# Performance work log

Measured on AMD Instinct MI355X. Metric: run time of the kernel, lower is better.

## Reference

```python
import jax, jax.numpy as jnp
import numpy as np

EMBED = 384
HEADS = 7
HEAD_SIZE = EMBED // HEADS  # 54; concat dim = 378 != 384 (faithful to source)
SEQ = 512
BATCH = 64
FFN = 6 * EMBED
EPS = 1e-5


def _layernorm(x, g, b):
    mu = jnp.mean(x, axis=-1, keepdims=True)
    var = jnp.mean((x - mu) ** 2, axis=-1, keepdims=True)
    return (x - mu) * jax.lax.rsqrt(var + EPS) * g + b


def setup_inputs() -> dict:
    key = jax.random.key(0)
    ks = jax.random.split(key, 14)
    s = 0.02
    return {
        "x": jax.random.normal(ks[0], (BATCH, SEQ, EMBED), jnp.float32),
        # per-head q/k/v projections stacked over heads: [H, EMBED, HEAD_SIZE]
        "wq": jax.random.normal(ks[1], (HEADS, EMBED, HEAD_SIZE), jnp.float32) * s,
        "bq": jnp.zeros((HEADS, HEAD_SIZE), jnp.float32),
        "wk": jax.random.normal(ks[2], (HEADS, EMBED, HEAD_SIZE), jnp.float32) * s,
        "bk": jnp.zeros((HEADS, HEAD_SIZE), jnp.float32),
        "wv": jax.random.normal(ks[3], (HEADS, EMBED, HEAD_SIZE), jnp.float32) * s,
        "bv": jnp.zeros((HEADS, HEAD_SIZE), jnp.float32),
        "wo": jax.random.normal(ks[4], (HEADS * HEAD_SIZE, EMBED), jnp.float32) * s,
        "bo": jnp.zeros((EMBED,), jnp.float32),
        "w1": jax.random.normal(ks[5], (EMBED, FFN), jnp.float32) * s,
        "b1": jnp.zeros((FFN,), jnp.float32),
        "w2": jax.random.normal(ks[6], (FFN, EMBED), jnp.float32) * s,
        "b2": jnp.zeros((EMBED,), jnp.float32),
        "ln1_g": jnp.ones((EMBED,), jnp.float32),
        "ln1_b": jnp.zeros((EMBED,), jnp.float32),
        "ln2_g": jnp.ones((EMBED,), jnp.float32),
        "ln2_b": jnp.zeros((EMBED,), jnp.float32),
    }


def reference(x, wq, bq, wk, bk, wv, bv, wo, bo, w1, b1, w2, b2, ln1_g, ln1_b, ln2_g, ln2_b):
    B, S, D = x.shape
    # --- multi-head causal self-attention (pre-LN) ---
    h = _layernorm(x, ln1_g, ln1_b)
    q = jnp.einsum("bsd,hdk->bhsk", h, wq) + bq[None, :, None, :]
    k = jnp.einsum("bsd,hdk->bhsk", h, wk) + bk[None, :, None, :]
    v = jnp.einsum("bsd,hdk->bhsk", h, wv) + bv[None, :, None, :]
    scale = HEAD_SIZE ** -0.5
    scores = jnp.einsum("bhsk,bhtk->bhst", q, k) * scale  # [B,H,S,S]
    causal = jnp.tril(jnp.ones((S, S), dtype=bool))
    scores = jnp.where(causal, scores, jnp.float32(-jnp.inf))
    attn = jax.nn.softmax(scores, axis=-1)
    o = jnp.einsum("bhst,bhtk->bhsk", attn, v)  # [B,H,S,hs]
    o = jnp.transpose(o, (0, 2, 1, 3)).reshape(B, S, HEADS * HEAD_SIZE)
    x = x + o @ wo + bo  # dropout = identity (eval)
    # --- feed-forward (pre-LN), exact GELU ---
    h2 = _layernorm(x, ln2_g, ln2_b)
    ff = jax.nn.gelu(h2 @ w1 + b1, approximate=False) @ w2 + b2
    return x + ff
```

## Files before the change

### kernel.cpp

```cpp
#include <hip/hip_runtime.h>
#include <hip/hip_bf16.h>
#include <cmath>

#define BATCH 64
#define SEQ   512
#define EMBED 384
#define HEADS 7
#define HSZ   54
#define FFND  2304
#define NTOK  (BATCH*SEQ)
#define QKVN  1152
#define EPS   1e-5f
#define SCALE 0.13608276348795434f

typedef __attribute__((ext_vector_type(8))) short s16x8;
typedef __attribute__((ext_vector_type(4))) float f32x4;

__device__ __forceinline__ ushort f2bf(float f) {
  __hip_bfloat16 h = __float2bfloat16(f);
  return *reinterpret_cast<ushort*>(&h);
}

__device__ __forceinline__ void gload16(const void* g, void* l) {
  __builtin_amdgcn_global_load_lds((const __attribute__((address_space(1))) void*)g,
                                   (__attribute__((address_space(3))) void*)l, 16, 0, 0);
}

__global__ __launch_bounds__(256) void ln_bf16_kernel(const float* __restrict__ x,
    const float* __restrict__ g, const float* __restrict__ b, ushort* __restrict__ out) {
  int wave = threadIdx.x >> 6, lane = threadIdx.x & 63;
  int row = (blockIdx.x << 2) + wave;
  const float* xr = x + (size_t)row * EMBED;
  float v[6]; float s = 0.f;
#pragma unroll
  for (int i = 0; i < 6; ++i) { v[i] = xr[lane + (i << 6)]; s += v[i]; }
#pragma unroll
  for (int off = 32; off; off >>= 1) s += __shfl_xor(s, off);
  float mu = s * (1.f / EMBED);
  float var = 0.f;
#pragma unroll
  for (int i = 0; i < 6; ++i) { float d = v[i] - mu; var += d * d; }
#pragma unroll
  for (int off = 32; off; off >>= 1) var += __shfl_xor(var, off);
  float rstd = rsqrtf(var * (1.f / EMBED) + EPS);
  ushort* orow = out + (size_t)row * EMBED;
#pragma unroll
  for (int i = 0; i < 6; ++i) {
    int c = lane + (i << 6);
    orow[c] = f2bf((v[i] - mu) * rstd * g[c] + b[c]);
  }
}

__global__ __launch_bounds__(256) void convT_tiled(const float* __restrict__ in,
    ushort* __restrict__ out, int K, int N, int srcK, int srcN) {
  __shared__ float t[32][33];
  int k0 = blockIdx.x << 5, n0 = blockIdx.y << 5;
  int tx = threadIdx.x & 31, ty = threadIdx.x >> 5;
#pragma unroll
  for (int i = 0; i < 4; ++i) {
    int r = ty + i * 8;
    int k = k0 + r, n = n0 + tx;
    t[r][tx] = (k < srcK && n < srcN) ? in[(size_t)k * srcN + n] : 0.f;
  }
  __syncthreads();
#pragma unroll
  for (int i = 0; i < 4; ++i) {
    int r = ty + i * 8;
    int n = n0 + r, k = k0 + tx;
    if (n < N && k < K) out[(size_t)n * K + k] = f2bf(t[tx][r]);
  }
}

__global__ __launch_bounds__(256) void conv_qkvw_tiled(const float* __restrict__ wq,
    const float* __restrict__ wk, const float* __restrict__ wv, ushort* __restrict__ wt) {
  __shared__ float t[32][33];
  int k0 = blockIdx.x << 5, hs0 = blockIdx.y << 5;
  int z = blockIdx.z, type = z / 7, h = z - type * 7;
  const float* W = (type == 0) ? wq : (type == 1) ? wk : wv;
  int tx = threadIdx.x & 31, ty = threadIdx.x >> 5;
#pragma unroll
  for (int i = 0; i < 4; ++i) {
    int r = ty + i * 8;
    int k = k0 + r, hs = hs0 + tx;
    t[r][tx] = (hs < HSZ) ? W[((size_t)h * EMBED + k) * HSZ + hs] : 0.f;
  }
  __syncthreads();
#pragma unroll
  for (int i = 0; i < 4; ++i) {
    int r = ty + i * 8;
    int hs = hs0 + r, k = k0 + tx;
    if (hs < HSZ) wt[(size_t)(type * 378 + h * HSZ + hs) * EMBED + k0 + tx] = f2bf(t[tx][r]);
  }
}

__global__ __launch_bounds__(256) void fill_misc(const float* __restrict__ bq,
    const float* __restrict__ bk, const float* __restrict__ bv,
    ushort* __restrict__ wt, float* __restrict__ bqkv) {
  int idx = blockIdx.x * 256 + threadIdx.x;
  if (idx < 18 * EMBED) wt[1134 * EMBED + idx] = 0;
  if (idx < QKVN) {
    float bval = 0.f;
    if (idx < 1134) {
      int type = idx / 378, rem = idx - type * 378;
      int h = rem / HSZ, hs = rem - h * HSZ;
      const float* B = (type == 0) ? bq : (type == 1) ? bk : bv;
      bval = B[h * HSZ + hs];
    }
    bqkv[idx] = bval;
  }
}

__global__ __launch_bounds__(256) void pad_aout_kernel(ushort* __restrict__ aout) {
  int idx = blockIdx.x * 256 + threadIdx.x;
  if (idx >= NTOK * 6) return;
  int row = idx / 6, c = idx - row * 6;
  aout[(size_t)row * EMBED + 378 + c] = 0;
}

__global__ __launch_bounds__(256) void attn_mfma_kernel(const ushort* __restrict__ qkv,
    ushort* __restrict__ o) {
  __shared__ ushort Ks[2][4096];
  __shared__ ushort Vt[2][4096];
  int tid = threadIdx.x;
  int id = blockIdx.x;
  int xcd = id & 7;
  int sseq = id >> 3;
  int bh = xcd + 8 * (sseq >> 3);
  int qt = (SEQ / 64 - 1) - (sseq & 7);
  int b = bh / HEADS, h = bh - b * HEADS;
  int qr0 = qt << 6;
  int w = tid >> 6, l = tid & 63;
  int lr = l & 15, lg = l >> 4;
  const ushort* base = qkv + (size_t)b * SEQ * QKVN + h * HSZ;
  const size_t TSTR = (size_t)64 * QKVN * 2;

  int grow = w * 8 + (l >> 3);
  int gc = (l & 7) ^ (l >> 3);
  const char* kg0 = (const char*)(base + 378 + (size_t)grow * QKVN + gc * 8);
  const char* kg1 = (const char*)(base + 378 + (size_t)(grow + 32) * QKVN + gc * 8);
  const char* qg0 = (const char*)(base + (size_t)(qr0 + grow) * QKVN + gc * 8);
  const char* qg1 = (const char*)(base + (size_t)(qr0 + grow + 32) * QKVN + gc * 8);
  int vdst[7]; const char* vsrc[7]; bool vpar[7];
#pragma unroll
  for (int i = 0; i < 7; ++i) {
    int e = tid + i * 256;
    int ev = e >> 1, par = e & 1;
    int p = ev / 28, cv = ev - p * 28;
    if (cv < 27) {
      int k0 = 2 * p;
      int s0 = ((k0 >> 5) << 5) | (((k0 >> 2) & 3) << 3) | (((k0 >> 4) & 1) << 2) | (k0 & 3);
      int d = 2 * cv + par;
      vdst[i] = d * 64 + (s0 ^ ((d & 7) << 3));
      vsrc[i] = (const char*)(base + 756 + (size_t)(2 * p + par) * QKVN + 2 * cv);
      vpar[i] = (par != 0);
    } else { vdst[i] = -1; vsrc[i] = (const char*)base; vpar[i] = false; }
  }

  gload16(qg0, (char*)&Ks[1][0] + w * 1024);
  gload16(qg1, (char*)&Ks[1][0] + 4096 + w * 1024);
  gload16(kg0, (char*)&Ks[0][0] + w * 1024);
  gload16(kg1, (char*)&Ks[0][0] + 4096 + w * 1024);
  uint uv[7];
#pragma unroll
  for (int i = 0; i < 7; ++i)
    uv[i] = (vdst[i] >= 0) ? *reinterpret_cast<const uint*>(vsrc[i]) : 0u;
  __syncthreads();
  for (int e = tid; e < 320; e += 256) {
    int r = e / 5, which = e - r * 5;
    int idx = (which == 0) ? (r * 64 + ((6 ^ (r & 7)) << 3) + 6)
                           : (r * 64 + ((7 ^ (r & 7)) << 3) + 2 * (which - 1));
    *reinterpret_cast<uint*>(&Ks[1][idx]) = 0;
  }
#pragma unroll
  for (int i = 0; i < 7; ++i) {
    uint u = uv[i]; uint uo = __shfl_xor(u, 1);
    if (vdst[i] >= 0) {
      uint wv2 = vpar[i] ? ((uo >> 16) | (u & 0xffff0000u)) : ((u & 0xffffu) | (uo << 16));
      *reinterpret_cast<uint*>(&Vt[0][vdst[i]]) = wv2;
    }
  }
  __syncthreads();
  int qrow = w * 16 + lr;
  s16x8 qf[2];
  qf[0] = *reinterpret_cast<const s16x8*>(&Ks[1][qrow * 64 + ((8 * lg) ^ ((qrow & 7) << 3))]);
  qf[1] = *reinterpret_cast<const s16x8*>(&Ks[1][qrow * 64 + ((32 + 8 * lg) ^ ((qrow & 7) << 3))]);
  __syncthreads();

  int qglob = qr0 + qrow;
  float mrow = -1e30f, lrow = 0.f;
  f32x4 acc[4];
#pragma unroll
  for (int d = 0; d < 4; ++d) acc[d] = (f32x4){0.f, 0.f, 0.f, 0.f};

  for (int kt = 0; kt <= qt; ++kt) {
    int cur = kt & 1, nxt = cur ^ 1;
    if (kt < qt) {
      kg0 += TSTR; kg1 += TSTR;
      gload16(kg0, (char*)&Ks[nxt][0] + w * 1024);
      gload16(kg1, (char*)&Ks[nxt][0] + 4096 + w * 1024);
#pragma unroll
      for (int i = 0; i < 7; ++i) {
        vsrc[i] += TSTR;
        if (vdst[i] >= 0) uv[i] = *reinterpret_cast<const uint*>(vsrc[i]);
      }
    }
    f32x4 sacc[4];
    __builtin_amdgcn_s_setprio(1);
#pragma unroll
    for (int kb = 0; kb < 4; ++kb) {
      sacc[kb] = (f32x4){0.f, 0.f, 0.f, 0.f};
#pragma unroll
      for (int h2 = 0; h2 < 2; ++h2) {
        int row = kb * 16 + lr;
        s16x8 kf = *reinterpret_cast<const s16x8*>(
            &Ks[cur][row * 64 + ((32 * h2 + 8 * lg) ^ ((row & 7) << 3))]);
        sacc[kb] = __builtin_amdgcn_mfma_f32_16x16x32_bf16(kf, qf[h2], sacc[kb], 0, 0, 0);
      }
    }
    __builtin_amdgcn_s_setprio(0);
    float sv[4][4];
    float mt = -1e30f;
    bool diag = (kt == qt);
#pragma unroll
    for (int kb = 0; kb < 4; ++kb)
#pragma unroll
      for (int r = 0; r < 4; ++r) {
        float s = sacc[kb][r] * SCALE;
        if (diag && (kt * 64 + kb * 16 + 4 * lg + r) > qglob) s = -1e30f;
        sv[kb][r] = s;
        mt = fmaxf(mt, s);
      }
    mt = fmaxf(mt, __shfl_xor(mt, 16));
    mt = fmaxf(mt, __shfl_xor(mt, 32));
    if (!__all(mt - mrow <= 8.f)) {
      float mnew = fmaxf(mrow, mt);
      float al = __expf(mrow - mnew);
#pragma unroll
      for (int d = 0; d < 4; ++d)
#pragma unroll
        for (int r = 0; r < 4; ++r) acc[d][r] *= al;
      lrow *= al;
      mrow = mnew;
    }
    union { short s[16]; s16x8 v[2]; } pp;
    float lsum = 0.f;
#pragma unroll
    for (int kb = 0; kb < 4; ++kb)
#pragma unroll
      for (int r = 0; r < 4; ++r) {
        float p = __expf(sv[kb][r] - mrow);
        lsum += p;
        pp.s[kb * 4 + r] = (short)f2bf(p);
      }
    lrow += lsum;
    __builtin_amdgcn_s_setprio(1);
#pragma unroll
    for (int m = 0; m < 2; ++m)
#pragma unroll
      for (int d = 0; d < 4; ++d) {
        int row = d * 16 + lr;
        s16x8 vf = *reinterpret_cast<const s16x8*>(
            &Vt[cur][row * 64 + ((32 * m + 8 * lg) ^ ((row & 7) << 3))]);
        acc[d] = __builtin_amdgcn_mfma_f32_16x16x32_bf16(vf, pp.v[m], acc[d], 0, 0, 0);
      }
    __builtin_amdgcn_s_setprio(0);
    if (kt < qt) {
#pragma unroll
      for (int i = 0; i < 7; ++i) {
        uint u = uv[i]; uint uo = __shfl_xor(u, 1);
        if (vdst[i] >= 0) {
          uint wv2 = vpar[i] ? ((uo >> 16) | (u & 0xffff0000u)) : ((u & 0xffffu) | (uo << 16));
          *reinterpret_cast<uint*>(&Vt[nxt][vdst[i]]) = wv2;
        }
      }
      __syncthreads();
    }
  }

  lrow += __shfl_xor(lrow, 16);
  lrow += __shfl_xor(lrow, 32);
  float linv = 1.f / lrow;
  __syncthreads();
  ushort* Olds = &Ks[0][0];
#pragma unroll
  for (int d = 0; d < 4; ++d)
#pragma unroll
    for (int r = 0; r < 4; ++r)
      Olds[(d * 16 + 4 * lg + r) * 64 + w * 16 + lr] = f2bf(acc[d][r] * linv);
  __syncthreads();
  for (int e = tid; e < 64 * 27; e += 256) {
    int q = e / 27, c = e - q * 27;
    uint lo = Olds[(2 * c) * 64 + q];
    uint hi = Olds[(2 * c + 1) * 64 + q];
    *reinterpret_cast<uint*>(&o[(size_t)(b * SEQ + qr0 + q) * EMBED + h * HSZ + 2 * c]) =
        lo | (hi << 16);
  }
}

template<int KSTEPS, int LDA, int LDB, int MODE, int NY>
__global__ __launch_bounds__(256) void mfma_gemm(
    const char* __restrict__ Ab, const char* __restrict__ Btb,
    const float* __restrict__ bias, const float* __restrict__ resid,
    char* __restrict__ Cb, int ncols) {
  __shared__ ushort sh[32768];
  int tid = threadIdx.x;
  int id = blockIdx.x;
  int xcd = id & 7, t = id >> 3;
  int group = t / (4 * NY), rres = t - group * (4 * NY);
  int ytile = rres >> 2, xi = rres & 3;
  int tok0 = (xcd * 32 + group * 4 + xi) << 7;
  int col0 = ytile << 7;
  int wv = tid >> 6, l = tid & 63;
  int wr = wv >> 1, wc = wv & 1;
  int lr = l & 15, lg = l >> 4;

  const char* aptr[4]; const char* bptr[4];
#pragma unroll
  for (int is = 0; is < 4; ++is) {
    int i = is * 256 + tid;
    int row = i >> 3;
    int boff = (i & 7) << 4;
    int sw = boff ^ ((row & 7) << 4);
    aptr[is] = Ab + (size_t)(tok0 + row) * LDA + sw;
    bptr[is] = Btb + (size_t)(col0 + row) * LDB + sw;
  }

  int offA[2][4], offB[2][4];
#pragma unroll
  for (int m = 0; m < 4; ++m) {
    int rowa = wr * 64 + m * 16 + lr;
    int rowb = wc * 64 + m * 16 + lr;
    int sa = (rowa & 7) << 4, sb = (rowb & 7) << 4;
#pragma unroll
    for (int kk = 0; kk < 2; ++kk) {
      int kb = kk * 64 + lg * 16;
      offA[kk][m] = (rowa * 128 + (kb ^ sa)) >> 1;
      offB[kk][m] = (rowb * 128 + (kb ^ sb)) >> 1;
    }
  }

  f32x4 acc[4][4];
#pragma unroll
  for (int m = 0; m < 4; ++m)
#pragma unroll
    for (int n = 0; n < 4; ++n) acc[m][n] = (f32x4){0.f, 0.f, 0.f, 0.f};

#pragma unroll
  for (int is = 0; is < 4; ++is) {
    gload16(aptr[is], (char*)sh + is * 4096 + wv * 1024);
    gload16(bptr[is], (char*)sh + 32768 + is * 4096 + wv * 1024);
  }
  __syncthreads();

  for (int ks = 0; ks < KSTEPS; ++ks) {
    int buf = ks & 1;
    if (ks + 1 < KSTEPS) {
      int nb = buf ^ 1;
#pragma unroll
      for (int is = 0; is < 4; ++is) {
        gload16(aptr[is] + (size_t)(ks + 1) * 128, (char*)sh + nb * 16384 + is * 4096 + wv * 1024);
        gload16(bptr[is] + (size_t)(ks + 1) * 128, (char*)sh + 32768 + nb * 16384 + is * 4096 + wv * 1024);
      }
    }
    int ao = buf * 8192, bo = 16384 + buf * 8192;
    __builtin_amdgcn_s_setprio(1);
#pragma unroll
    for (int kk = 0; kk < 2; ++kk) {
      s16x8 af[4], bfr[4];
#pragma unroll
      for (int m = 0; m < 4; ++m) af[m] = *reinterpret_cast<const s16x8*>(&sh[ao + offA[kk][m]]);
#pragma unroll
      for (int n = 0; n < 4; ++n) bfr[n] = *reinterpret_cast<const s16x8*>(&sh[bo + offB[kk][n]]);
#pragma unroll
      for (int m = 0; m < 4; ++m)
#pragma unroll
        for (int n = 0; n < 4; ++n)
          acc[m][n] = __builtin_amdgcn_mfma_f32_16x16x32_bf16(af[m], bfr[n], acc[m][n], 0, 0, 0);
    }
    __builtin_amdgcn_s_setprio(0);
    if (ks + 1 < KSTEPS) __syncthreads();
  }

  float bn[4];
  int colr = col0 + wc * 64 + lr;
#pragma unroll
  for (int n = 0; n < 4; ++n) bn[n] = bias[colr + n * 16];

  if constexpr (MODE == 2) {
    int tokr = tok0 + wr * 64 + lg * 4;
    float* C = (float*)Cb;
#pragma unroll
    for (int m = 0; m < 4; ++m)
#pragma unroll
      for (int r = 0; r < 4; ++r) {
        size_t rowbase = (size_t)(tokr + m * 16 + r) * ncols;
#pragma unroll
        for (int n = 0; n < 4; ++n) {
          size_t idx = rowbase + colr + n * 16;
          C[idx] = acc[m][n][r] + bn[n] + resid[idx];
        }
      }
  } else {
    __syncthreads();
#pragma unroll
    for (int m = 0; m < 4; ++m)
#pragma unroll
      for (int r = 0; r < 4; ++r) {
        int row = wr * 64 + m * 16 + lg * 4 + r;
        int rmask = ((row >> 2) & 3) << 4;
#pragma unroll
        for (int n = 0; n < 4; ++n) {
          float xg = acc[m][n][r] + bn[n];
          if constexpr (MODE == 1) {
            float u2 = xg * (1.5957691216f + 0.0713548162f * xg * xg);
            xg = xg * __builtin_amdgcn_rcpf(1.f + __expf(-u2));
          }
          int col = wc * 64 + n * 16 + lr;
          sh[row * 128 + (col ^ rmask)] = f2bf(xg);
        }
      }
    __syncthreads();
    ushort* C = (ushort*)Cb;
    int blk = (l & 7) + 8 * (wv & 1);
    int rbase = (l >> 3) + 64 * (wv >> 1);
#pragma unroll
    for (int it = 0; it < 8; ++it) {
      int row = rbase + 8 * it;
      int pblk = blk ^ (((row >> 2) & 3) << 1);
      uint4 vvv = *reinterpret_cast<const uint4*>(&sh[row * 128 + pblk * 8]);
      *reinterpret_cast<uint4*>(&C[(size_t)(tok0 + row) * ncols + col0 + blk * 8]) = vvv;
    }
  }
}

extern "C" void kernel_launch(void* const* d_in, const int* in_sizes, int n_in,
                              void* d_out, int out_size, void* d_ws, size_t ws_size,
                              hipStream_t stream) {
  const float* x    = (const float*)d_in[0];
  const float* wq   = (const float*)d_in[1];
  const float* bq   = (const float*)d_in[2];
  const float* wk   = (const float*)d_in[3];
  const float* bk   = (const float*)d_in[4];
  const float* wv   = (const float*)d_in[5];
  const float* bv   = (const float*)d_in[6];
  const float* wo   = (const float*)d_in[7];
  const float* bo   = (const float*)d_in[8];
  const float* w1   = (const float*)d_in[9];
  const float* b1   = (const float*)d_in[10];
  const float* w2   = (const float*)d_in[11];
  const float* b2   = (const float*)d_in[12];
  const float* ln1g = (const float*)d_in[13];
  const float* ln1b = (const float*)d_in[14];
  const float* ln2g = (const float*)d_in[15];
  const float* ln2b = (const float*)d_in[16];
  float* out = (float*)d_out;

  char* wsb = (char*)d_ws;
  float*  x1    = (float*)wsb;
  ushort* ffnb  = (ushort*)(wsb + 50331648);
  ushort* hb    = (ushort*)(wsb + 50331648);
  ushort* qkvb  = (ushort*)(wsb + 75497472);
  ushort* aout  = (ushort*)(wsb + 150994944);
  ushort* h2b   = (ushort*)(wsb + 201326592);
  ushort* w1t   = (ushort*)(wsb + 226492416);
  ushort* w2t   = (ushort*)(wsb + 228261888);
  ushort* wqkvt = (ushort*)(wsb + 230031360);
  ushort* wot   = (ushort*)(wsb + 230916096);
  float*  bqkv  = (float*)(wsb + 231211008);

  conv_qkvw_tiled<<<dim3(12, 2, 21), 256, 0, stream>>>(wq, wk, wv, wqkvt);
  fill_misc      <<<27, 256, 0, stream>>>(bq, bk, bv, wqkvt, bqkv);
  convT_tiled    <<<dim3(12, 12), 256, 0, stream>>>(wo, wot, EMBED, EMBED, 378, EMBED);
  convT_tiled    <<<dim3(12, 72), 256, 0, stream>>>(w1, w1t, EMBED, FFND, EMBED, FFND);
  convT_tiled    <<<dim3(72, 12), 256, 0, stream>>>(w2, w2t, FFND, EMBED, FFND, EMBED);
  pad_aout_kernel<<<(NTOK * 6 + 255) / 256, 256, 0, stream>>>(aout);

  ln_bf16_kernel<<<NTOK / 4, 256, 0, stream>>>(x, ln1g, ln1b, hb);
  mfma_gemm<EMBED / 64, EMBED * 2, EMBED * 2, 0, QKVN / 128>
      <<<256 * (QKVN / 128), 256, 0, stream>>>(
      (const char*)hb, (const char*)wqkvt, bqkv, nullptr, (char*)qkvb, QKVN);
  attn_mfma_kernel<<<BATCH * HEADS * (SEQ / 64), 256, 0, stream>>>(qkvb, aout);
  mfma_gemm<EMBED / 64, EMBED * 2, EMBED * 2, 2, EMBED / 128>
      <<<256 * (EMBED / 128), 256, 0, stream>>>(
      (const char*)aout, (const char*)wot, bo, x, (char*)x1, EMBED);
  ln_bf16_kernel<<<NTOK / 4, 256, 0, stream>>>(x1, ln2g, ln2b, h2b);
  mfma_gemm<EMBED / 64, EMBED * 2, EMBED * 2, 1, FFND / 128>
      <<<256 * (FFND / 128), 256, 0, stream>>>(
      (const char*)h2b, (const char*)w1t, b1, nullptr, (char*)ffnb, FFND);
  mfma_gemm<FFND / 64, FFND * 2, FFND * 2, 2, EMBED / 128>
      <<<256 * (EMBED / 128), 256, 0, stream>>>(
      (const char*)ffnb, (const char*)w2t, b2, x1, (char*)out, EMBED);
}
```

Before: 385.8 us.

## Use 128-row query blocks with 512-thread attention blocks sharing K/V tiles

Each attention block now handles 128 query rows with 8 waves instead of 64 rows with 4 waves, so every K/V tile loaded into shared memory serves twice as many queries. Q moves to its own LDS buffer, and waves whose rows lie entirely before a key tile skip that tile's compute. This halves global K/V traffic per query and the number of blocks. In exchange it adds some causal imbalance between waves inside a block and uses more LDS and threads per block, which may lower occupancy.

New measurement: 383.0 us. No clear change (-0.7%).

```diff
diff --git a/kernel.cpp b/kernel.cpp
--- a/kernel.cpp
+++ b/kernel.cpp
@@ -117,18 +117,20 @@
   aout[(size_t)row * EMBED + 378 + c] = 0;
 }
 
-__global__ __launch_bounds__(256) void attn_mfma_kernel(const ushort* __restrict__ qkv,
+__global__ __launch_bounds__(512) void attn_mfma_kernel(const ushort* __restrict__ qkv,
     ushort* __restrict__ o) {
+  __shared__ ushort Qsh[8192];
   __shared__ ushort Ks[2][4096];
   __shared__ ushort Vt[2][4096];
   int tid = threadIdx.x;
   int id = blockIdx.x;
   int xcd = id & 7;
   int sseq = id >> 3;
-  int bh = xcd + 8 * (sseq >> 3);
-  int qt = (SEQ / 64 - 1) - (sseq & 7);
+  int bh = xcd + 8 * (sseq >> 2);
+  int qb = 3 - (sseq & 3);
   int b = bh / HEADS, h = bh - b * HEADS;
-  int qr0 = qt << 6;
+  int qr0 = qb << 7;
+  int ntile = 2 * qb + 2;
   int w = tid >> 6, l = tid & 63;
   int lr = l & 15, lg = l >> 4;
   const ushort* base = qkv + (size_t)b * SEQ * QKVN + h * HSZ;
@@ -136,17 +138,16 @@
 
   int grow = w * 8 + (l >> 3);
   int gc = (l & 7) ^ (l >> 3);
-  const char* kg0 = (const char*)(base + 378 + (size_t)grow * QKVN + gc * 8);
-  const char* kg1 = (const char*)(base + 378 + (size_t)(grow + 32) * QKVN + gc * 8);
+  const char* kg  = (const char*)(base + 378 + (size_t)grow * QKVN + gc * 8);
   const char* qg0 = (const char*)(base + (size_t)(qr0 + grow) * QKVN + gc * 8);
-  const char* qg1 = (const char*)(base + (size_t)(qr0 + grow + 32) * QKVN + gc * 8);
-  int vdst[7]; const char* vsrc[7]; bool vpar[7];
-#pragma unroll
-  for (int i = 0; i < 7; ++i) {
-    int e = tid + i * 256;
+  const char* qg1 = (const char*)(base + (size_t)(qr0 + 64 + grow) * QKVN + gc * 8);
+  int vdst[4]; const char* vsrc[4]; bool vpar[4];
+#pragma unroll
+  for (int i = 0; i < 4; ++i) {
+    int e = tid + i * 512;
     int ev = e >> 1, par = e & 1;
     int p = ev / 28, cv = ev - p * 28;
-    if (cv < 27) {
+    if (cv < 27 && p < 32) {
       int k0 = 2 * p;
       int s0 = ((k0 >> 5) << 5) | (((k0 >> 2) & 3) << 3) | (((k0 >> 4) & 1) << 2) | (k0 & 3);
       int d = 2 * cv + par;
@@ -156,23 +157,22 @@
     } else { vdst[i] = -1; vsrc[i] = (const char*)base; vpar[i] = false; }
   }
 
-  gload16(qg0, (char*)&Ks[1][0] + w * 1024);
-  gload16(qg1, (char*)&Ks[1][0] + 4096 + w * 1024);
-  gload16(kg0, (char*)&Ks[0][0] + w * 1024);
-  gload16(kg1, (char*)&Ks[0][0] + 4096 + w * 1024);
-  uint uv[7];
-#pragma unroll
-  for (int i = 0; i < 7; ++i)
+  gload16(qg0, (char*)Qsh + w * 1024);
+  gload16(qg1, (char*)Qsh + 8192 + w * 1024);
+  gload16(kg, (char*)&Ks[0][0] + w * 1024);
+  uint uv[4];
+#pragma unroll
+  for (int i = 0; i < 4; ++i)
     uv[i] = (vdst[i] >= 0) ? *reinterpret_cast<const uint*>(vsrc[i]) : 0u;
   __syncthreads();
-  for (int e = tid; e < 320; e += 256) {
+  for (int e = tid; e < 640; e += 512) {
     int r = e / 5, which = e - r * 5;
     int idx = (which == 0) ? (r * 64 + ((6 ^ (r & 7)) << 3) + 6)
                            : (r * 64 + ((7 ^ (r & 7)) << 3) + 2 * (which - 1));
-    *reinterpret_cast<uint*>(&Ks[1][idx]) = 0;
-  }
-#pragma unroll
-  for (int i = 0; i < 7; ++i) {
+    *reinterpret_cast<uint*>(&Qsh[idx]) = 0;
+  }
+#pragma unroll
+  for (int i = 0; i < 4; ++i) {
     uint u = uv[i]; uint uo = __shfl_xor(u, 1);
     if (vdst[i] >= 0) {
       uint wv2 = vpar[i] ? ((uo >> 16) | (u & 0xffff0000u)) : ((u & 0xffffu) | (uo << 16));
@@ -182,9 +182,8 @@
   __syncthreads();
   int qrow = w * 16 + lr;
   s16x8 qf[2];
-  qf[0] = *reinterpret_cast<const s16x8*>(&Ks[1][qrow * 64 + ((8 * lg) ^ ((qrow & 7) << 3))]);
-  qf[1] = *reinterpret_cast<const s16x8*>(&Ks[1][qrow * 64 + ((32 + 8 * lg) ^ ((qrow & 7) << 3))]);
-  __syncthreads();
+  qf[0] = *reinterpret_cast<const s16x8*>(&Qsh[qrow * 64 + ((8 * lg) ^ ((qrow & 7) << 3))]);
+  qf[1] = *reinterpret_cast<const s16x8*>(&Qsh[qrow * 64 + ((32 + 8 * lg) ^ ((qrow & 7) << 3))]);
 
   int qglob = qr0 + qrow;
   float mrow = -1e30f, lrow = 0.f;
@@ -192,81 +191,83 @@
 #pragma unroll
   for (int d = 0; d < 4; ++d) acc[d] = (f32x4){0.f, 0.f, 0.f, 0.f};
 
-  for (int kt = 0; kt <= qt; ++kt) {
+  for (int kt = 0; kt < ntile; ++kt) {
     int cur = kt & 1, nxt = cur ^ 1;
-    if (kt < qt) {
-      kg0 += TSTR; kg1 += TSTR;
-      gload16(kg0, (char*)&Ks[nxt][0] + w * 1024);
-      gload16(kg1, (char*)&Ks[nxt][0] + 4096 + w * 1024);
-#pragma unroll
-      for (int i = 0; i < 7; ++i) {
+    if (kt + 1 < ntile) {
+      kg += TSTR;
+      gload16(kg, (char*)&Ks[nxt][0] + w * 1024);
+#pragma unroll
+      for (int i = 0; i < 4; ++i) {
         vsrc[i] += TSTR;
         if (vdst[i] >= 0) uv[i] = *reinterpret_cast<const uint*>(vsrc[i]);
       }
     }
-    f32x4 sacc[4];
-    __builtin_amdgcn_s_setprio(1);
-#pragma unroll
-    for (int kb = 0; kb < 4; ++kb) {
-      sacc[kb] = (f32x4){0.f, 0.f, 0.f, 0.f};
-#pragma unroll
-      for (int h2 = 0; h2 < 2; ++h2) {
-        int row = kb * 16 + lr;
-        s16x8 kf = *reinterpret_cast<const s16x8*>(
-            &Ks[cur][row * 64 + ((32 * h2 + 8 * lg) ^ ((row & 7) << 3))]);
-        sacc[kb] = __builtin_amdgcn_mfma_f32_16x16x32_bf16(kf, qf[h2], sacc[kb], 0, 0, 0);
-      }
-    }
-    __builtin_amdgcn_s_setprio(0);
-    float sv[4][4];
-    float mt = -1e30f;
-    bool diag = (kt == qt);
-#pragma unroll
-    for (int kb = 0; kb < 4; ++kb)
-#pragma unroll
-      for (int r = 0; r < 4; ++r) {
-        float s = sacc[kb][r] * SCALE;
-        if (diag && (kt * 64 + kb * 16 + 4 * lg + r) > qglob) s = -1e30f;
-        sv[kb][r] = s;
-        mt = fmaxf(mt, s);
-      }
-    mt = fmaxf(mt, __shfl_xor(mt, 16));
-    mt = fmaxf(mt, __shfl_xor(mt, 32));
-    if (!__all(mt - mrow <= 8.f)) {
-      float mnew = fmaxf(mrow, mt);
-      float al = __expf(mrow - mnew);
-#pragma unroll
-      for (int d = 0; d < 4; ++d)
-#pragma unroll
-        for (int r = 0; r < 4; ++r) acc[d][r] *= al;
-      lrow *= al;
-      mrow = mnew;
-    }
-    union { short s[16]; s16x8 v[2]; } pp;
-    float lsum = 0.f;
-#pragma unroll
-    for (int kb = 0; kb < 4; ++kb)
-#pragma unroll
-      for (int r = 0; r < 4; ++r) {
-        float p = __expf(sv[kb][r] - mrow);
-        lsum += p;
-        pp.s[kb * 4 + r] = (short)f2bf(p);
-      }
-    lrow += lsum;
-    __builtin_amdgcn_s_setprio(1);
-#pragma unroll
-    for (int m = 0; m < 2; ++m)
-#pragma unroll
-      for (int d = 0; d < 4; ++d) {
-        int row = d * 16 + lr;
-        s16x8 vf = *reinterpret_cast<const s16x8*>(
-            &Vt[cur][row * 64 + ((32 * m + 8 * lg) ^ ((row & 7) << 3))]);
-        acc[d] = __builtin_amdgcn_mfma_f32_16x16x32_bf16(vf, pp.v[m], acc[d], 0, 0, 0);
-      }
-    __builtin_amdgcn_s_setprio(0);
-    if (kt < qt) {
-#pragma unroll
-      for (int i = 0; i < 7; ++i) {
+    bool active = (kt * 64) <= (qr0 + w * 16 + 15);
+    if (active) {
+      bool diag = (kt * 64 + 63) > (qr0 + w * 16);
+      f32x4 sacc[4];
+      __builtin_amdgcn_s_setprio(1);
+#pragma unroll
+      for (int kb = 0; kb < 4; ++kb) {
+        sacc[kb] = (f32x4){0.f, 0.f, 0.f, 0.f};
+#pragma unroll
+        for (int h2 = 0; h2 < 2; ++h2) {
+          int row = kb * 16 + lr;
+          s16x8 kf = *reinterpret_cast<const s16x8*>(
+              &Ks[cur][row * 64 + ((32 * h2 + 8 * lg) ^ ((row & 7) << 3))]);
+          sacc[kb] = __builtin_amdgcn_mfma_f32_16x16x32_bf16(kf, qf[h2], sacc[kb], 0, 0, 0);
+        }
+      }
+      __builtin_amdgcn_s_setprio(0);
+      float sv[4][4];
+      float mt = -1e30f;
+#pragma unroll
+      for (int kb = 0; kb < 4; ++kb)
+#pragma unroll
+        for (int r = 0; r < 4; ++r) {
+          float s = sacc[kb][r] * SCALE;
+          if (diag && (kt * 64 + kb * 16 + 4 * lg + r) > qglob) s = -1e30f;
+          sv[kb][r] = s;
+          mt = fmaxf(mt, s);
+        }
+      mt = fmaxf(mt, __shfl_xor(mt, 16));
+      mt = fmaxf(mt, __shfl_xor(mt, 32));
+      if (!__all(mt - mrow <= 8.f)) {
+        float mnew = fmaxf(mrow, mt);
+        float al = __expf(mrow - mnew);
+#pragma unroll
+        for (int d = 0; d < 4; ++d)
+#pragma unroll
+          for (int r = 0; r < 4; ++r) acc[d][r] *= al;
+        lrow *= al;
+        mrow = mnew;
+      }
+      union { short s[16]; s16x8 v[2]; } pp;
+      float lsum = 0.f;
+#pragma unroll
+      for (int kb = 0; kb < 4; ++kb)
+#pragma unroll
+        for (int r = 0; r < 4; ++r) {
+          float p = __expf(sv[kb][r] - mrow);
+          lsum += p;
+          pp.s[kb * 4 + r] = (short)f2bf(p);
+        }
+      lrow += lsum;
+      __builtin_amdgcn_s_setprio(1);
+#pragma unroll
+      for (int m = 0; m < 2; ++m)
+#pragma unroll
+        for (int d = 0; d < 4; ++d) {
+          int row = d * 16 + lr;
+          s16x8 vf = *reinterpret_cast<const s16x8*>(
+              &Vt[cur][row * 64 + ((32 * m + 8 * lg) ^ ((row & 7) << 3))]);
+          acc[d] = __builtin_amdgcn_mfma_f32_16x16x32_bf16(vf, pp.v[m], acc[d], 0, 0, 0);
+        }
+      __builtin_amdgcn_s_setprio(0);
+    }
+    if (kt + 1 < ntile) {
+#pragma unroll
+      for (int i = 0; i < 4; ++i) {
         uint u = uv[i]; uint uo = __shfl_xor(u, 1);
         if (vdst[i] >= 0) {
           uint wv2 = vpar[i] ? ((uo >> 16) | (u & 0xffff0000u)) : ((u & 0xffffu) | (uo << 16));
@@ -280,18 +281,17 @@
   lrow += __shfl_xor(lrow, 16);
   lrow += __shfl_xor(lrow, 32);
   float linv = 1.f / lrow;
-  __syncthreads();
-  ushort* Olds = &Ks[0][0];
+  ushort* Olds = Qsh;
 #pragma unroll
   for (int d = 0; d < 4; ++d)
 #pragma unroll
     for (int r = 0; r < 4; ++r)
-      Olds[(d * 16 + 4 * lg + r) * 64 + w * 16 + lr] = f2bf(acc[d][r] * linv);
-  __syncthreads();
-  for (int e = tid; e < 64 * 27; e += 256) {
+      Olds[(d * 16 + 4 * lg + r) * 128 + w * 16 + lr] = f2bf(acc[d][r] * linv);
+  __syncthreads();
+  for (int e = tid; e < 128 * 27; e += 512) {
     int q = e / 27, c = e - q * 27;
-    uint lo = Olds[(2 * c) * 64 + q];
-    uint hi = Olds[(2 * c + 1) * 64 + q];
+    uint lo = Olds[(2 * c) * 128 + q];
+    uint hi = Olds[(2 * c + 1) * 128 + q];
     *reinterpret_cast<uint*>(&o[(size_t)(b * SEQ + qr0 + q) * EMBED + h * HSZ + 2 * c]) =
         lo | (hi << 16);
   }
@@ -479,7 +479,7 @@
   mfma_gemm<EMBED / 64, EMBED * 2, EMBED * 2, 0, QKVN / 128>
       <<<256 * (QKVN / 128), 256, 0, stream>>>(
       (const char*)hb, (const char*)wqkvt, bqkv, nullptr, (char*)qkvb, QKVN);
-  attn_mfma_kernel<<<BATCH * HEADS * (SEQ / 64), 256, 0, stream>>>(qkvb, aout);
+  attn_mfma_kernel<<<BATCH * HEADS * 4, 512, 0, stream>>>(qkvb, aout);
   mfma_gemm<EMBED / 64, EMBED * 2, EMBED * 2, 2, EMBED / 128>
       <<<256 * (EMBED / 128), 256, 0, stream>>>(
       (const char*)aout, (const char*)wot, bo, x, (char*)x1, EMBED);
```
